# Kernel tuning notes

Hardware: AMD Instinct MI355X
Metric: run time of the kernel (lower is better)

Reference implementation:

```python
import jax, jax.numpy as jnp
import numpy as np

D_MODEL = 4096
D_FIBER = 64
D_LATENT = 512
OMEGA = 0.1
B, L = 4, 4096


def cayley(A):
    # Q = (I - A)^{-1} (I + A), batched over leading dim; A is skew-symmetric
    d = A.shape[-1]
    I = jnp.eye(d, dtype=A.dtype)
    return jnp.linalg.solve(I - A, I + A)


def setup_inputs() -> dict:
    key = jax.random.key(0)
    k1, k2, k3, k4, k5 = jax.random.split(key, 5)
    h_t = jax.random.normal(k1, (B, L, D_MODEL), dtype=jnp.float32)
    z0 = jax.random.normal(k2, (B, D_LATENT), dtype=jnp.float32)
    A_raw = jax.random.normal(k3, (B, D_FIBER, D_FIBER), dtype=jnp.float32) * 0.1
    A_u = A_raw - jnp.swapaxes(A_raw, -1, -2)  # skew-symmetric gauge connection
    # frozen projection weights, torch nn.Linear layout: (out_features, in_features)
    W_down = jax.random.normal(k4, (D_FIBER, D_MODEL), dtype=jnp.float32) / np.sqrt(D_MODEL)
    W_up = jax.random.normal(k5, (D_MODEL, D_FIBER), dtype=jnp.float32) / np.sqrt(D_FIBER)
    alpha = jnp.float32(OMEGA)
    return {"h_t": h_t, "z0": z0, "A_u": A_u, "alpha": alpha, "W_down": W_down, "W_up": W_up}


def reference(h_t, z0, A_u, alpha, W_down, W_up):
    # psi_down: (B,L,d_model) @ (d_model,d_fiber)
    h_fiber = jnp.einsum('bld,fd->blf', h_t, W_down)
    Q_u = cayley(A_u)  # (B, d_fiber, d_fiber)
    # h_fiber @ Q_u^T per batch
    h_rot = jnp.einsum('blf,bgf->blg', h_fiber, Q_u)
    delta = h_rot - h_fiber
    h_out = h_t + alpha * jnp.einsum('blf,df->bld', delta, W_up)
    return h_out
```

## Files before the change

kernel.cpp:

```cpp
#include <hip/hip_runtime.h>
#include <hip/hip_bf16.h>
#include <cstdint>

#define D_MODEL 4096
#define NFIB    64
#define NBATCH  4
#define LSEQ    4096
#define NTOK    (NBATCH * LSEQ)
#define NSL     8

typedef __attribute__((ext_vector_type(4))) float f32x4;
typedef __attribute__((ext_vector_type(8))) short bf16x8;

__device__ __forceinline__ unsigned short f2bf(float f) {
  unsigned int u = __builtin_bit_cast(unsigned int, f);
  u += 0x7FFFu + ((u >> 16) & 1u);
  return (unsigned short)(u >> 16);
}

__device__ __forceinline__ bf16x8 cvt8(f32x4 a, f32x4 b) {
  union { __hip_bfloat162 h2[4]; bf16x8 v; } u;
  u.h2[0] = __float22bfloat162_rn(make_float2(a[0], a[1]));
  u.h2[1] = __float22bfloat162_rn(make_float2(a[2], a[3]));
  u.h2[2] = __float22bfloat162_rn(make_float2(b[0], b[1]));
  u.h2[3] = __float22bfloat162_rn(make_float2(b[2], b[3]));
  return u.v;
}

__device__ __forceinline__ void addbf8(f32x4& x0, f32x4& x1, bf16x8 v) {
#pragma unroll
  for (int j = 0; j < 4; ++j)
    x0[j] += __builtin_bit_cast(float, (uint32_t)(unsigned short)v[j] << 16);
#pragma unroll
  for (int j = 0; j < 4; ++j)
    x1[j] += __builtin_bit_cast(float, (uint32_t)(unsigned short)v[j + 4] << 16);
}

__global__ __launch_bounds__(256) void prep1_kernel(const float* __restrict__ A,
                                                    const float* __restrict__ Wd,
                                                    float* __restrict__ S,
                                                    unsigned short* __restrict__ Wd2) {
  const int blk = blockIdx.x;
  if (blk >= NBATCH) {
    int idx = (blk - NBATCH) * 256 + threadIdx.x;
    int j    = idx & 7;
    int lane = (idx >> 3) & 63;
    int nf   = (idx >> 9) & 3;
    int ks   = idx >> 11;
    int row = nf * 16 + (lane & 15);
    int col = ks * 32 + (lane >> 4) * 8 + j;
    Wd2[idx] = f2bf(Wd[row * D_MODEL + col]);
    return;
  }
  __shared__ float M[64][66];
  __shared__ float R[64][66];
  const int b = blk;
  const int tid = threadIdx.x;
  const int k = tid & 63;
  const int g = tid >> 6;
  const float* Ab = A + b * 4096;
#pragma unroll
  for (int ii = 0; ii < 16; ++ii) {
    int i = g * 16 + ii;
    float a = Ab[i * 64 + k];
    M[i][k] = ((i == k) ? 1.0f : 0.0f) - a;
    R[i][k] = 2.0f * a;
  }
  for (int j = 0; j < 64; ++j) {
    __syncthreads();
    float pr  = 1.0f / M[j][j];
    float mjk = M[j][k], rjk = R[j][k];
    float f[16];
#pragma unroll
    for (int ii = 0; ii < 16; ++ii) f[ii] = M[g * 16 + ii][j] * pr;
    __syncthreads();
#pragma unroll
    for (int ii = 0; ii < 16; ++ii) {
      int i = g * 16 + ii;
      if (i != j) { M[i][k] -= f[ii] * mjk; R[i][k] -= f[ii] * rjk; }
    }
  }
  __syncthreads();
  float* Sb = S + b * 4096;
#pragma unroll
  for (int ii = 0; ii < 16; ++ii) {
    int i = g * 16 + ii;
    Sb[i * 64 + k] = R[i][k] / M[i][i];
  }
}

__global__ __launch_bounds__(256) void prep_u_kernel(const float* __restrict__ Wup,
                                                     const float* __restrict__ S,
                                                     const float* __restrict__ alpha_p,
                                                     unsigned short* __restrict__ U2) {
  __shared__ float Sl[4096];
  const int blk = blockIdx.x;
  const int b = blk >> 7;
  const int ntg = blk & 127;
  const float* Sb = S + b * 4096;
  for (int i = threadIdx.x; i < 1024; i += 256)
    ((f32x4*)Sl)[i] = ((const f32x4*)Sb)[i];
  __syncthreads();

  const int t = threadIdx.x;
  const int nt   = ntg * 2 + (t >> 7);
  const int h    = (t >> 6) & 1;
  const int lane = t & 63;
  const int d = nt * 16 + (lane & 15);
  const int fbase = h * 32 + (lane >> 4) * 8;
  const float alpha = alpha_p[0];
  const f32x4* wr = (const f32x4*)(Wup + d * 64);

  float s[8];
#pragma unroll
  for (int j = 0; j < 8; ++j) s[j] = 0.f;
#pragma unroll
  for (int g4 = 0; g4 < 16; ++g4) {
    f32x4 wv = wr[g4];
#pragma unroll
    for (int gg = 0; gg < 4; ++gg) {
      const float* srow = &Sl[(g4 * 4 + gg) * 64 + fbase];
      float wvg = wv[gg];
#pragma unroll
      for (int j = 0; j < 8; ++j) s[j] += wvg * srow[j];
    }
  }
  bf16x8 v;
#pragma unroll
  for (int j = 0; j < 8; ++j) v[j] = (short)f2bf(alpha * s[j]);
  *(bf16x8*)(U2 + ((((size_t)b * 256 + nt) * 64 + lane) * 2 + h) * 8) = v;
}

__global__ __launch_bounds__(256, 4) void p1_kernel(
    const float* __restrict__ H, const unsigned short* __restrict__ Wd2,
    unsigned short* __restrict__ Fpb) {
  const int blk = blockIdx.x;
  const int tg = blk >> 3;
  const int ks = blk & 7;
  const int tid = threadIdx.x;
  const int w = tid >> 6, l = tid & 63, lr = l & 15, lq = l >> 4;

  const int rowW = tg * 64 + w * 16;
  const float* ha = H + (size_t)(rowW + lr) * D_MODEL + ks * 512 + lq * 8;
  const unsigned short* wb = Wd2 + (((size_t)(ks * 16) * 4) * 64 + l) * 8;

  f32x4 acc[4];
#pragma unroll
  for (int nf = 0; nf < 4; ++nf) acc[nf] = (f32x4){0, 0, 0, 0};

  for (int s = 0; s < 16; ++s) {
    const float* hp = ha + s * 32;
    f32x4 a0 = *(const f32x4*)hp;
    f32x4 a1 = *(const f32x4*)(hp + 4);
    bf16x8 afr = cvt8(a0, a1);
    const unsigned short* wp = wb + (size_t)s * 2048;
#pragma unroll
    for (int nf = 0; nf < 4; ++nf) {
      bf16x8 bfr = *(const bf16x8*)(wp + (size_t)nf * 512);
      acc[nf] = __builtin_amdgcn_mfma_f32_16x16x32_bf16(afr, bfr, acc[nf], 0, 0, 0);
    }
  }

  unsigned short* fp = Fpb + (size_t)ks * (NTOK * 64);
#pragma unroll
  for (int nf = 0; nf < 4; ++nf)
#pragma unroll
    for (int rr = 0; rr < 4; ++rr)
      fp[(size_t)(rowW + lq * 4 + rr) * 64 + nf * 16 + lr] = f2bf(acc[nf][rr]);
}

__global__ __launch_bounds__(256, 8) void pf_kernel(
    const unsigned short* __restrict__ Fpb, unsigned short* __restrict__ F2) {
  const int idx = blockIdx.x * 256 + threadIdx.x;
  const size_t off = (size_t)idx * 8;
  f32x4 x0 = {0, 0, 0, 0}, x1 = {0, 0, 0, 0};
#pragma unroll
  for (int ks = 0; ks < NSL; ++ks)
    addbf8(x0, x1, *(const bf16x8*)(Fpb + (size_t)ks * (NTOK * 64) + off));
  *(bf16x8*)(F2 + off) = cvt8(x0, x1);
}

__global__ __launch_bounds__(256, 4) void p2_kernel(
    const float* __restrict__ H, const unsigned short* __restrict__ F2,
    const unsigned short* __restrict__ U2, float* __restrict__ Out) {
  const int blk = blockIdx.x;
  const int tg = blk >> 4;
  const int cc = blk & 15;
  const int rowB = tg * 64;
  const int b = rowB >> 12;
  const int tid = threadIdx.x;
  const int w = tid >> 6, l = tid & 63, lr = l & 15, lq = l >> 4;

  const int colW = cc * 256 + w * 64;
  const int nt0 = colW >> 4;

  const unsigned short* ub = U2 + (((size_t)b * 256 + nt0) * 64 + l) * 16;
  bf16x8 u0[4], u1[4];
#pragma unroll
  for (int nt = 0; nt < 4; ++nt) {
    u0[nt] = *(const bf16x8*)(ub + (size_t)nt * 1024);
    u1[nt] = *(const bf16x8*)(ub + (size_t)nt * 1024 + 8);
  }

  bf16x8 fb0[4], fb1[4];
#pragma unroll
  for (int g = 0; g < 4; ++g) {
    const unsigned short* fp = F2 + (size_t)(rowB + g * 16 + lr) * 64 + lq * 8;
    fb0[g] = *(const bf16x8*)fp;
    fb1[g] = *(const bf16x8*)(fp + 32);
  }

#pragma unroll
  for (int g = 0; g < 4; ++g) {
    const size_t rbase = (size_t)(rowB + g * 16 + lr) * D_MODEL + colW + lq * 4;
#pragma unroll
    for (int nt = 0; nt < 4; ++nt) {
      f32x4 hr = *(const f32x4*)(H + rbase + nt * 16);
      f32x4 c = {0, 0, 0, 0};
      c = __builtin_amdgcn_mfma_f32_16x16x32_bf16(u0[nt], fb0[g], c, 0, 0, 0);
      c = __builtin_amdgcn_mfma_f32_16x16x32_bf16(u1[nt], fb1[g], c, 0, 0, 0);
      *(f32x4*)(Out + rbase + nt * 16) = hr + c;
    }
  }
}

extern "C" void kernel_launch(void* const* d_in, const int* in_sizes, int n_in,
                              void* d_out, int out_size, void* d_ws, size_t ws_size,
                              hipStream_t stream) {
  const float* h_t    = (const float*)d_in[0];
  const float* A_u    = (const float*)d_in[2];
  const float* alpha  = (const float*)d_in[3];
  const float* W_down = (const float*)d_in[4];
  const float* W_up   = (const float*)d_in[5];
  float* out = (float*)d_out;

  char* ws = (char*)d_ws;
  float*          S   = (float*)ws;
  unsigned short* Wd2 = (unsigned short*)(ws + (64 << 10));
  unsigned short* U2  = (unsigned short*)(ws + (576 << 10));
  unsigned short* Fpb = (unsigned short*)(ws + (2624 << 10));
  unsigned short* F2  = (unsigned short*)(ws + (19008 << 10));

  prep1_kernel<<<NBATCH + 1024, 256, 0, stream>>>(A_u, W_down, S, Wd2);
  prep_u_kernel<<<512, 256, 0, stream>>>(W_up, S, alpha, U2);
  p1_kernel<<<2048, 256, 0, stream>>>(h_t, Wd2, Fpb);
  pf_kernel<<<512, 256, 0, stream>>>(Fpb, F2);
  p2_kernel<<<4096, 256, 0, stream>>>(h_t, F2, U2, out);
}
```

Before: 270.8 us.

## Coalesce H loads and output stores via per-wave LDS transpose in p1/p2

Both passes now read 64-float-wide row segments of H with fully coalesced 16-lane row loads, and stage them through a per-wave shared-memory tile that converts to the MFMA fragment layout. Before, each lane read strided 32-byte pieces across rows. In p1 the staged tile feeds the A fragments. In p2 the MFMA results are written to LDS and re-read in row-contiguous order, so the residual add and the output store are coalesced. p2 is also retiled to 16 rows by 1024 columns per block, which reloads U fragments per subtile instead of keeping them in registers. The cost is extra LDS traffic and more U2 reads, in exchange for better DRAM access patterns in this memory-bound workload.

After: 280.8 us. 1.04x slower.

```diff
diff --git a/kernel.cpp b/kernel.cpp
--- a/kernel.cpp
+++ b/kernel.cpp
@@ -140,24 +140,39 @@
   const int tid = threadIdx.x;
   const int w = tid >> 6, l = tid & 63, lr = l & 15, lq = l >> 4;
 
+  __shared__ float T[4][16][68];
+  float (*Tw)[68] = T[w];
+
   const int rowW = tg * 64 + w * 16;
-  const float* ha = H + (size_t)(rowW + lr) * D_MODEL + ks * 512 + lq * 8;
-  const unsigned short* wb = Wd2 + (((size_t)(ks * 16) * 4) * 64 + l) * 8;
+  const int g16 = l >> 4;
+  const int c16 = (l & 15) * 4;
 
   f32x4 acc[4];
 #pragma unroll
   for (int nf = 0; nf < 4; ++nf) acc[nf] = (f32x4){0, 0, 0, 0};
 
-  for (int s = 0; s < 16; ++s) {
-    const float* hp = ha + s * 32;
-    f32x4 a0 = *(const f32x4*)hp;
-    f32x4 a1 = *(const f32x4*)(hp + 4);
-    bf16x8 afr = cvt8(a0, a1);
-    const unsigned short* wp = wb + (size_t)s * 2048;
-#pragma unroll
-    for (int nf = 0; nf < 4; ++nf) {
-      bf16x8 bfr = *(const bf16x8*)(wp + (size_t)nf * 512);
-      acc[nf] = __builtin_amdgcn_mfma_f32_16x16x32_bf16(afr, bfr, acc[nf], 0, 0, 0);
+  for (int ch = 0; ch < 8; ++ch) {
+    const int colb = ks * 512 + ch * 64;
+    f32x4 hv[4];
+#pragma unroll
+    for (int i = 0; i < 4; ++i)
+      hv[i] = *(const f32x4*)(H + (size_t)(rowW + 4 * i + g16) * D_MODEL + colb + c16);
+#pragma unroll
+    for (int i = 0; i < 4; ++i)
+      *(f32x4*)&Tw[4 * i + g16][c16] = hv[i];
+
+#pragma unroll
+    for (int h = 0; h < 2; ++h) {
+      f32x4 p0 = *(const f32x4*)&Tw[lr][h * 32 + lq * 8];
+      f32x4 p1v = *(const f32x4*)&Tw[lr][h * 32 + lq * 8 + 4];
+      bf16x8 afr = cvt8(p0, p1v);
+      const int sg = ks * 16 + ch * 2 + h;
+      const unsigned short* wp = Wd2 + (((size_t)sg * 4) * 64 + l) * 8;
+#pragma unroll
+      for (int nf = 0; nf < 4; ++nf) {
+        bf16x8 bfr = *(const bf16x8*)(wp + (size_t)nf * 512);
+        acc[nf] = __builtin_amdgcn_mfma_f32_16x16x32_bf16(afr, bfr, acc[nf], 0, 0, 0);
+      }
     }
   }
 
@@ -184,42 +199,47 @@
     const float* __restrict__ H, const unsigned short* __restrict__ F2,
     const unsigned short* __restrict__ U2, float* __restrict__ Out) {
   const int blk = blockIdx.x;
-  const int tg = blk >> 4;
-  const int cc = blk & 15;
-  const int rowB = tg * 64;
-  const int b = rowB >> 12;
+  const int tile = blk >> 2;
+  const int cc4 = blk & 3;
+  const int row0 = tile * 16;
+  const int b = tile >> 8;
   const int tid = threadIdx.x;
   const int w = tid >> 6, l = tid & 63, lr = l & 15, lq = l >> 4;
 
-  const int colW = cc * 256 + w * 64;
-  const int nt0 = colW >> 4;
-
-  const unsigned short* ub = U2 + (((size_t)b * 256 + nt0) * 64 + l) * 16;
-  bf16x8 u0[4], u1[4];
-#pragma unroll
-  for (int nt = 0; nt < 4; ++nt) {
-    u0[nt] = *(const bf16x8*)(ub + (size_t)nt * 1024);
-    u1[nt] = *(const bf16x8*)(ub + (size_t)nt * 1024 + 8);
-  }
-
-  bf16x8 fb0[4], fb1[4];
-#pragma unroll
-  for (int g = 0; g < 4; ++g) {
-    const unsigned short* fp = F2 + (size_t)(rowB + g * 16 + lr) * 64 + lq * 8;
-    fb0[g] = *(const bf16x8*)fp;
-    fb1[g] = *(const bf16x8*)(fp + 32);
-  }
-
-#pragma unroll
-  for (int g = 0; g < 4; ++g) {
-    const size_t rbase = (size_t)(rowB + g * 16 + lr) * D_MODEL + colW + lq * 4;
+  __shared__ float T[4][16][68];
+  float (*Tw)[68] = T[w];
+
+  const int g16 = l >> 4;
+  const int c16 = (l & 15) * 4;
+
+  const unsigned short* fp = F2 + (size_t)(row0 + lr) * 64 + lq * 8;
+  bf16x8 fb0 = *(const bf16x8*)fp;
+  bf16x8 fb1 = *(const bf16x8*)(fp + 32);
+
+  for (int sub = 0; sub < 4; ++sub) {
+    const int colb = cc4 * 1024 + w * 256 + sub * 64;
+    const int nt0 = colb >> 4;
+
+    f32x4 hv[4];
+#pragma unroll
+    for (int i = 0; i < 4; ++i)
+      hv[i] = *(const f32x4*)(H + (size_t)(row0 + 4 * i + g16) * D_MODEL + colb + c16);
+
+    const unsigned short* ub = U2 + (((size_t)b * 256 + nt0) * 64 + l) * 16;
 #pragma unroll
     for (int nt = 0; nt < 4; ++nt) {
-      f32x4 hr = *(const f32x4*)(H + rbase + nt * 16);
+      bf16x8 u0 = *(const bf16x8*)(ub + (size_t)nt * 1024);
+      bf16x8 u1 = *(const bf16x8*)(ub + (size_t)nt * 1024 + 8);
       f32x4 c = {0, 0, 0, 0};
-      c = __builtin_amdgcn_mfma_f32_16x16x32_bf16(u0[nt], fb0[g], c, 0, 0, 0);
-      c = __builtin_amdgcn_mfma_f32_16x16x32_bf16(u1[nt], fb1[g], c, 0, 0, 0);
-      *(f32x4*)(Out + rbase + nt * 16) = hr + c;
+      c = __builtin_amdgcn_mfma_f32_16x16x32_bf16(u0, fb0, c, 0, 0, 0);
+      c = __builtin_amdgcn_mfma_f32_16x16x32_bf16(u1, fb1, c, 0, 0, 0);
+      *(f32x4*)&Tw[lr][nt * 16 + lq * 4] = c;
+    }
+
+#pragma unroll
+    for (int i = 0; i < 4; ++i) {
+      f32x4 cv = *(const f32x4*)&Tw[4 * i + g16][c16];
+      *(f32x4*)(Out + (size_t)(row0 + 4 * i + g16) * D_MODEL + colb + c16) = hv[i] + cv;
     }
   }
 }
```
